# Kernel tuning notes

Hardware: AMD Instinct MI355X
Metric: run time of the kernel (lower is better)

The kernel has to match this reference:

```python
import jax, jax.numpy as jnp
import numpy as np

OUT = 7          # roi_align output_size
NUM_ANCHORS = 27 # 3 scales x 3 ratios x 3 angles
MAX_PROPOSALS = 100
RPN_STRIDE = 32


def conv2d(x, w, b, stride=1, pad=1):
    y = jax.lax.conv_general_dilated(
        x, w, (stride, stride), [(pad, pad), (pad, pad)],
        dimension_numbers=('NCHW', 'OIHW', 'NCHW'))
    return y + b[None, :, None, None]


def generate_anchors(H, W, stride):
    # matches CustomOrientedRPN.generate_anchors
    sx = np.arange(0, W * stride, stride, dtype=np.float32)
    sy = np.arange(0, H * stride, stride, dtype=np.float32)
    SY, SX = np.meshgrid(sy, sx, indexing='ij')
    shifts = np.stack([SX, SY], axis=-1).reshape(-1, 2)  # [HW,2]
    base = []
    for scale in (32.0, 64.0, 128.0):
        for ratio in (0.5, 1.0, 2.0):
            w = scale * ratio ** 0.5
            h = scale / ratio ** 0.5
            for angle in (0.0, 45.0, 90.0):
                base.append([w, h, angle])
    base = np.array(base, dtype=np.float32)  # [A,3]
    A = base.shape[0]
    anchors = np.concatenate(
        [np.repeat(shifts[:, None, :], A, axis=1),
         np.broadcast_to(base[None], (shifts.shape[0], A, 3))], axis=-1)
    return jnp.asarray(anchors.reshape(-1, 5))  # [HW*A, 5]


def rotated_roi_align(features, boxes, batch_idx):
    # Vectorized version of the per-box affine_grid + grid_sample loop
    # (align_corners=False semantics for both, zero padding for grid_sample).
    B, C, Hf, Wf = features.shape
    lin = (2.0 * jnp.arange(OUT, dtype=features.dtype) + 1.0) / OUT - 1.0
    ys, xs = jnp.meshgrid(lin, lin, indexing='ij')  # [7,7] base grid

    cx, cy, w, h, ang = (boxes[:, i] for i in range(5))
    ar = -ang * jnp.pi / 180.0
    c, s = jnp.cos(ar), jnp.sin(ar)
    t00 = w / Wf * c; t01 = -h / Hf * s; t02 = 2.0 * cx / Wf - 1.0
    t10 = w / Wf * s; t11 = h / Hf * c;  t12 = 2.0 * cy / Hf - 1.0
    gx = t00[:, None, None] * xs + t01[:, None, None] * ys + t02[:, None, None]  # [N,7,7]
    gy = t10[:, None, None] * xs + t11[:, None, None] * ys + t12[:, None, None]

    ix = ((gx + 1.0) * Wf - 1.0) / 2.0
    iy = ((gy + 1.0) * Hf - 1.0) / 2.0
    x0 = jnp.floor(ix); y0 = jnp.floor(iy)
    wx = ix - x0;       wy = iy - y0
    x0i = x0.astype(jnp.int32); y0i = y0.astype(jnp.int32)

    def gather(dx, dy, wgt):
        xi = x0i + dx; yi = y0i + dy
        valid = (xi >= 0) & (xi < Wf) & (yi >= 0) & (yi < Hf)
        xc = jnp.clip(xi, 0, Wf - 1)
        yc = jnp.clip(yi, 0, Hf - 1)
        def one(bi, yb, xb):
            return features[bi][:, yb, xb]  # [C,7,7]
        vals = jax.vmap(one)(batch_idx, yc, xc)  # [N,C,7,7]
        return vals * (wgt * valid)[:, None, :, :]

    return (gather(0, 0, (1 - wx) * (1 - wy)) + gather(1, 0, wx * (1 - wy)) +
            gather(0, 1, (1 - wx) * wy) + gather(1, 1, wx * wy))


def setup_inputs() -> dict:
    key = jax.random.key(0)
    ks = jax.random.split(key, 20)

    def w(k, shape):
        fan_in = int(np.prod(shape[1:]))
        return jax.random.normal(k, shape, jnp.float32) / np.sqrt(fan_in)

    C = 256; A = NUM_ANCHORS; NC = 5
    return {
        'images': jax.random.normal(ks[0], (8, 3, 1024, 1024), jnp.float32),
        'backbone_w': w(ks[1], (C, 3, 3, 3)),   'backbone_b': jnp.zeros((C,), jnp.float32),
        'rpn_conv_w': w(ks[2], (256, C, 3, 3)), 'rpn_conv_b': jnp.zeros((256,), jnp.float32),
        'obj_w': w(ks[3], (A, 256, 1, 1)),      'obj_b': jnp.zeros((A,), jnp.float32),
        'delta_w': w(ks[4], (A * 5, 256, 1, 1)) * 0.1, 'delta_b': jnp.zeros((A * 5,), jnp.float32),
        'fc1_w': w(ks[5], (1024, C * OUT * OUT)), 'fc1_b': jnp.zeros((1024,), jnp.float32),
        'fc2_w': w(ks[6], (1024, 1024)),          'fc2_b': jnp.zeros((1024,), jnp.float32),
        'cls_w': w(ks[7], (NC, 1024)),            'cls_b': jnp.zeros((NC,), jnp.float32),
        'bbox_w': w(ks[8], (5, 1024)),            'bbox_b': jnp.zeros((5,), jnp.float32),
    }


def reference(images, backbone_w, backbone_b, rpn_conv_w, rpn_conv_b,
              obj_w, obj_b, delta_w, delta_b,
              fc1_w, fc1_b, fc2_w, fc2_b, cls_w, cls_b, bbox_w, bbox_b):
    # backbone (stand-in: single stride-16 conv)
    f = conv2d(images, backbone_w, backbone_b, stride=16, pad=1)  # [B,256,64,64]
    B, C, H, W = f.shape
    # F.interpolate(scale_factor=0.5, bilinear, align_corners=False) == 2x2 mean
    f = f.reshape(B, C, H // 2, 2, W // 2, 2).mean(axis=(3, 5))   # [B,256,32,32]
    Hf, Wf = f.shape[2], f.shape[3]

    # RPN
    t = jax.nn.relu(conv2d(f, rpn_conv_w, rpn_conv_b, 1, 1))
    _logits = conv2d(t, obj_w, obj_b, 1, 0)  # computed as in original (unused downstream)
    deltas = conv2d(t, delta_w, delta_b, 1, 0)  # [B, A*5, Hf, Wf]
    A = NUM_ANCHORS
    deltas = deltas.reshape(B, A, 5, Hf, Wf).transpose(0, 3, 4, 1, 2).reshape(B, -1, 5)

    anchors = generate_anchors(Hf, Wf, RPN_STRIDE)  # [HW*A,5]
    acx, acy, aw, ah, aa = (anchors[:, i] for i in range(5))
    pcx = deltas[:, :, 0] * aw + acx
    pcy = deltas[:, :, 1] * ah + acy
    pw = jnp.exp(deltas[:, :, 2]) * aw
    ph = jnp.exp(deltas[:, :, 3]) * ah
    pa = aa + deltas[:, :, 4]
    proposals = jnp.stack([pcx, pcy, pw, ph, pa], axis=-1)  # [B, HW*A, 5]
    proposals = proposals[:, :MAX_PROPOSALS]                # p[:max_proposals]

    boxes = proposals.reshape(-1, 5)                        # [B*100, 5]
    batch_idx = jnp.repeat(jnp.arange(B), MAX_PROPOSALS)
    pooled = rotated_roi_align(f, boxes, batch_idx)         # [B*100, 256, 7, 7]

    x = pooled.reshape(pooled.shape[0], -1)
    x = jax.nn.relu(x @ fc1_w.T + fc1_b)
    x = jax.nn.relu(x @ fc2_w.T + fc2_b)
    class_logits = x @ cls_w.T + cls_b
    obb_preds = x @ bbox_w.T + bbox_b
    return class_logits, obb_preds
```

## Files before the change

### kernel.cpp

```cpp
#include <hip/hip_runtime.h>
#include <hip/hip_bf16.h>

using bf16 = __hip_bfloat16;

typedef __attribute__((ext_vector_type(8))) short bf16x8;
typedef __attribute__((ext_vector_type(4))) float f32x4;

__device__ __forceinline__ void async16(const void* g, void* l) {
  __builtin_amdgcn_global_load_lds(
      (const __attribute__((address_space(1))) unsigned int*)g,
      (__attribute__((address_space(3))) unsigned int*)l, 16, 0, 0);
}

__device__ __forceinline__ void store_o(float* C, size_t i, float v) { C[i] = v; }
__device__ __forceinline__ void store_o(bf16* C, size_t i, float v) {
  C[i] = __float2bfloat16(v);
}

__global__ __launch_bounds__(256) void k_backbone(const float* __restrict__ img,
    const float* __restrict__ w, const float* __restrict__ bias,
    float* __restrict__ f) {
  int blk = blockIdx.x;
  int x = blk & 31, y = (blk >> 5) & 31, b = blk >> 10;
  __shared__ float patch[4 * 27];
  int t = threadIdx.x;
  if (t < 108) {
    int kx = t % 3, ky = (t / 3) % 3, cin = (t / 9) % 3, sub = t / 27;
    int sy = sub >> 1, sx = sub & 1;
    int iy = (2 * y + sy) * 16 - 1 + ky;
    int ix = (2 * x + sx) * 16 - 1 + kx;
    float v = 0.f;
    if (iy >= 0 && ix >= 0)
      v = img[((size_t)(b * 3 + cin) * 1024 + iy) * 1024 + ix];
    patch[t] = v;
  }
  __syncthreads();
  int c = t;
  float wr[27];
#pragma unroll
  for (int k = 0; k < 27; ++k) wr[k] = w[c * 27 + k];
  float acc = 0.f;
#pragma unroll
  for (int sub = 0; sub < 4; ++sub)
#pragma unroll
    for (int k = 0; k < 27; ++k)
      acc += patch[sub * 27 + k] * wr[k];
  f[(size_t)blk * 256 + c] = acc * 0.25f + bias[c];
}

__global__ __launch_bounds__(256) void k_rpn(const float* __restrict__ f,
    const float* __restrict__ rpn_w, float* __restrict__ part) {
  int p = blockIdx.x;
  int kc = blockIdx.y;
  int x = p & 3, b = p >> 2;
  __shared__ float fpl[6][16];
  int tid = threadIdx.x;
  if (tid < 96) {
    int cin2 = tid & 15;
    int rc = tid >> 4;
    int row = rc / 3, col = rc % 3;
    int xc = x - 1 + col;
    float v = 0.f;
    if (xc >= 0)
      v = f[((size_t)(b * 32 + row) * 32 + xc) * 256 + kc * 16 + cin2];
    fpl[rc][cin2] = v;
  }
  __syncthreads();
  int c = tid;
  const float* wbase = rpn_w + (size_t)c * 2304 + kc * 144;
  float acc = 0.f;
#pragma unroll
  for (int cin2 = 0; cin2 < 16; ++cin2) {
    const float* wp = wbase + cin2 * 9;
    acc += fpl[0][cin2] * wp[3] + fpl[1][cin2] * wp[4]
         + fpl[2][cin2] * wp[5] + fpl[3][cin2] * wp[6]
         + fpl[4][cin2] * wp[7] + fpl[5][cin2] * wp[8];
  }
  part[((size_t)kc * 32 + p) * 256 + c] = acc;
}

__global__ __launch_bounds__(512) void k_delta(const float* __restrict__ part,
    const float* __restrict__ rpn_b,
    const float* __restrict__ dw, const float* __restrict__ db,
    float* __restrict__ boxes) {
  int p = blockIdx.x;
  int x = p & 3, b = p >> 2;
  __shared__ float tbuf[256];
  __shared__ float dvals[135];
  int tid = threadIdx.x;
  if (tid < 256) {
    float s = rpn_b[tid];
#pragma unroll
    for (int kc = 0; kc < 16; ++kc)
      s += part[((size_t)kc * 32 + p) * 256 + tid];
    tbuf[tid] = fmaxf(s, 0.f);
  }
  __syncthreads();
  if (tid < 270) {
    int o = tid >> 1, half = tid & 1;
    const float* wp = dw + (size_t)o * 256 + half * 128;
    const float* tp = tbuf + half * 128;
    float s = 0.f;
#pragma unroll 8
    for (int k = 0; k < 128; ++k) s += tp[k] * wp[k];
    s += __shfl_xor(s, 1, 64);
    if (half == 0) dvals[o] = s + db[o];
  }
  __syncthreads();
  if (tid < 27) {
    int i = x * 27 + tid;
    if (i < 100) {
      int a = tid;
      int si = a / 9, ri = (a / 3) % 3, ai = a % 3;
      float scale = 32.f * (float)(1 << si);
      float sr = (ri == 0) ? 0.70710678118654752f : (ri == 1 ? 1.0f : 1.41421356237309505f);
      float aw = scale * sr, ah = scale / sr;
      float aang = 45.f * (float)ai;
      float acx = 32.f * (float)x, acy = 0.f;
      float* bx = boxes + (size_t)(b * 100 + i) * 5;
      bx[0] = dvals[a * 5 + 0] * aw + acx;
      bx[1] = dvals[a * 5 + 1] * ah + acy;
      bx[2] = expf(dvals[a * 5 + 2]) * aw;
      bx[3] = expf(dvals[a * 5 + 3]) * ah;
      bx[4] = aang + dvals[a * 5 + 4];
    }
  }
}

__global__ __launch_bounds__(256) void k_roialign(const float* __restrict__ f,
    const float* __restrict__ boxes, bf16* __restrict__ pooled) {
  int n = blockIdx.x;
  int b = n / 100;
  __shared__ int six[49], siy[49];
  __shared__ float swx[49], swy[49];
  __shared__ float pool_s[12544];
  int tid = threadIdx.x;
  if (tid < 49) {
    float cx = boxes[n * 5 + 0], cy = boxes[n * 5 + 1];
    float w = boxes[n * 5 + 2], h = boxes[n * 5 + 3], ang = boxes[n * 5 + 4];
    float ar = -ang * 0.017453292519943295f;
    float cc = cosf(ar), ss = sinf(ar);
    float t00 = w * (1.f / 32.f) * cc, t01 = -h * (1.f / 32.f) * ss;
    float t02 = cx * (2.f / 32.f) - 1.f;
    float t10 = w * (1.f / 32.f) * ss, t11 = h * (1.f / 32.f) * cc;
    float t12 = cy * (2.f / 32.f) - 1.f;
    int py = tid / 7, px = tid - py * 7;
    float lx = (2.f * px + 1.f) * (1.f / 7.f) - 1.f;
    float ly = (2.f * py + 1.f) * (1.f / 7.f) - 1.f;
    float gx = t00 * lx + t01 * ly + t02;
    float gy = t10 * lx + t11 * ly + t12;
    float ix = ((gx + 1.f) * 32.f - 1.f) * 0.5f;
    float iy = ((gy + 1.f) * 32.f - 1.f) * 0.5f;
    float x0 = floorf(ix), y0 = floorf(iy);
    six[tid] = (int)x0; siy[tid] = (int)y0;
    swx[tid] = ix - x0; swy[tid] = iy - y0;
  }
  __syncthreads();
  const float* fb = f + (size_t)b * 262144;
  int c = tid;
  for (int bin = 0; bin < 49; ++bin) {
    int x0 = six[bin], y0 = siy[bin];
    float wx = swx[bin], wy = swy[bin];
    float acc = 0.f;
    if (x0 >= 0 && x0 < 32 && y0 >= 0 && y0 < 32)
      acc += fb[(y0 * 32 + x0) * 256 + c] * ((1.f - wx) * (1.f - wy));
    if (x0 + 1 >= 0 && x0 + 1 < 32 && y0 >= 0 && y0 < 32)
      acc += fb[(y0 * 32 + x0 + 1) * 256 + c] * (wx * (1.f - wy));
    if (x0 >= 0 && x0 < 32 && y0 + 1 >= 0 && y0 + 1 < 32)
      acc += fb[((y0 + 1) * 32 + x0) * 256 + c] * ((1.f - wx) * wy);
    if (x0 + 1 >= 0 && x0 + 1 < 32 && y0 + 1 >= 0 && y0 + 1 < 32)
      acc += fb[((y0 + 1) * 32 + x0 + 1) * 256 + c] * (wx * wy);
    pool_s[c * 49 + bin] = acc;
  }
  __syncthreads();
  bf16* po = pooled + (size_t)n * 12544;
  for (int k = tid; k < 12544; k += 256) po[k] = __float2bfloat16(pool_s[k]);
}

__device__ __forceinline__ unsigned int pk2(float a, float b) {
  unsigned int ua = __bfloat16_as_ushort(__float2bfloat16(a));
  unsigned int ub = __bfloat16_as_ushort(__float2bfloat16(b));
  return ua | (ub << 16);
}
__global__ __launch_bounds__(256) void k_cvt(const float* __restrict__ s,
    uint2* __restrict__ d, int n4) {
  int stride = gridDim.x * 256;
  for (int j = blockIdx.x * 256 + threadIdx.x; j < n4; j += stride) {
    float4 v = ((const float4*)s)[j];
    uint2 o;
    o.x = pk2(v.x, v.y);
    o.y = pk2(v.z, v.w);
    d[j] = o;
  }
}

__global__ __launch_bounds__(256) void k_gemm_bb(
    const unsigned short* __restrict__ A, const unsigned short* __restrict__ B,
    float* __restrict__ P, int M, int N, int K, int KC) {
  __shared__ unsigned short As[128 * 64];
  __shared__ unsigned short Bs[128 * 64];
  int t = threadIdx.x;
  int wv = t >> 6, ln = t & 63;
  int quad = ln >> 4, l15 = ln & 15;
  int wm = wv >> 1, wn = wv & 1;
  int n0 = blockIdx.x * 128, m0 = blockIdx.y * 128;
  int kbeg = blockIdx.z * KC;
  int kend = kbeg + KC; if (kend > K) kend = K;

  int srow = ln >> 3;
  int sg = (ln & 7) ^ srow;
  const unsigned short* Ap[4];
#pragma unroll
  for (int q = 0; q < 4; ++q) {
    int r = m0 + q * 32 + wv * 8 + srow;
    if (r > M - 1) r = M - 1;
    Ap[q] = A + (size_t)r * K + sg * 8;
  }
  const unsigned short* Bp[4];
#pragma unroll
  for (int c = 0; c < 4; ++c) {
    int r = n0 + wv * 32 + c * 8 + srow;
    Bp[c] = B + (size_t)r * K + sg * 8;
  }

  f32x4 acc[4][4];
#pragma unroll
  for (int mf = 0; mf < 4; ++mf)
#pragma unroll
    for (int nf = 0; nf < 4; ++nf) acc[mf][nf] = (f32x4){0.f, 0.f, 0.f, 0.f};

  for (int k0 = kbeg; k0 < kend; k0 += 64) {
    __syncthreads();
#pragma unroll
    for (int q = 0; q < 4; ++q)
      async16(Ap[q] + k0, &As[q * 2048 + wv * 512]);
#pragma unroll
    for (int c = 0; c < 4; ++c)
      async16(Bp[c] + k0, &Bs[wv * 2048 + c * 512]);
    __syncthreads();
#pragma unroll
    for (int ks = 0; ks < 2; ++ks) {
      bf16x8 a[4];
#pragma unroll
      for (int mf = 0; mf < 4; ++mf) {
        int row = wm * 64 + mf * 16 + l15;
        a[mf] = *(const bf16x8*)&As[row * 64 + (((ks * 4 + quad) ^ (l15 & 7)) * 8)];
      }
#pragma unroll
      for (int nf = 0; nf < 4; ++nf) {
        int brow = wn * 64 + nf * 16 + l15;
        bf16x8 b = *(const bf16x8*)&Bs[brow * 64 + (((ks * 4 + quad) ^ (l15 & 7)) * 8)];
#pragma unroll
        for (int mf = 0; mf < 4; ++mf)
          acc[mf][nf] = __builtin_amdgcn_mfma_f32_16x16x32_bf16(a[mf], b, acc[mf][nf], 0, 0, 0);
      }
    }
  }
#pragma unroll
  for (int nf = 0; nf < 4; ++nf) {
    int n = n0 + wn * 64 + nf * 16 + l15;
#pragma unroll
    for (int mf = 0; mf < 4; ++mf) {
#pragma unroll
      for (int r = 0; r < 4; ++r) {
        int m = m0 + wm * 64 + mf * 16 + quad * 4 + r;
        if (m < M) atomicAdd(&P[(size_t)m * N + n], acc[mf][nf][r]);
      }
    }
  }
}

template <typename OutT>
__global__ __launch_bounds__(256) void k_bias_relu(const float* __restrict__ P,
    const float* __restrict__ bias, OutT* __restrict__ C, int MN, int N) {
  int i = blockIdx.x * 256 + threadIdx.x;
  if (i * 4 >= MN) return;
  f32x4 s = *(const f32x4*)(P + (size_t)i * 4);
  int n = (i * 4) % N;
#pragma unroll
  for (int u = 0; u < 4; ++u)
    store_o(C, (size_t)i * 4 + u, fmaxf(s[u] + bias[n + u], 0.f));
}

__global__ __launch_bounds__(640) void k_heads(const float* __restrict__ x2,
    const float* __restrict__ cls_w, const float* __restrict__ cls_b,
    const float* __restrict__ bbox_w, const float* __restrict__ bbox_b,
    float* __restrict__ out) {
  int n = blockIdx.x;
  int wave = threadIdx.x >> 6;
  int lane = threadIdx.x & 63;
  const float* w = (wave < 5) ? (cls_w + (size_t)wave * 1024)
                              : (bbox_w + (size_t)(wave - 5) * 1024);
  const float* xr = x2 + (size_t)n * 1024;
  float s = 0.f;
  for (int k = lane; k < 1024; k += 64) s += xr[k] * w[k];
  for (int off = 32; off; off >>= 1) s += __shfl_down(s, off, 64);
  if (lane == 0) {
    int o = (wave < 5) ? wave : wave - 5;
    float bias = (wave < 5) ? cls_b[o] : bbox_b[o];
    int base = (wave < 5) ? 0 : 4000;
    out[base + n * 5 + o] = s + bias;
  }
}

extern "C" void kernel_launch(void* const* d_in, const int* in_sizes, int n_in,
                              void* d_out, int out_size, void* d_ws, size_t ws_size,
                              hipStream_t stream) {
  const float* images     = (const float*)d_in[0];
  const float* backbone_w = (const float*)d_in[1];
  const float* backbone_b = (const float*)d_in[2];
  const float* rpn_w      = (const float*)d_in[3];
  const float* rpn_b      = (const float*)d_in[4];
  const float* delta_w    = (const float*)d_in[7];
  const float* delta_b    = (const float*)d_in[8];
  const float* fc1_w      = (const float*)d_in[9];
  const float* fc1_b      = (const float*)d_in[10];
  const float* fc2_w      = (const float*)d_in[11];
  const float* fc2_b      = (const float*)d_in[12];
  const float* cls_w      = (const float*)d_in[13];
  const float* cls_b      = (const float*)d_in[14];
  const float* bbox_w     = (const float*)d_in[15];
  const float* bbox_b     = (const float*)d_in[16];

  char* ws = (char*)d_ws;
  bf16*  bw1    = (bf16*) ws;
  float* f      = (float*)ws;
  float* boxes  = (float*)(ws + 25690112);
  bf16*  pooled = (bf16*) (ws + 25706496);
  float* x2     = (float*)(ws + 25706496);
  bf16*  x1     = (bf16*) (ws + 45776896);
  float* P      = (float*)(ws + 47415296);
  bf16*  bw2    = (bf16*) (ws + 50692096);
  float* rpart  = P;

  k_backbone<<<8192, 256, 0, stream>>>(images, backbone_w, backbone_b, f);
  k_rpn<<<dim3(32, 16), 256, 0, stream>>>(f, rpn_w, rpart);
  k_delta<<<32, 512, 0, stream>>>(rpart, rpn_b, delta_w, delta_b, boxes);
  k_roialign<<<800, 256, 0, stream>>>(f, boxes, pooled);

  k_cvt<<<2048, 256, 0, stream>>>(fc1_w, (uint2*)bw1, 3211264);
  k_cvt<<<512, 256, 0, stream>>>(fc2_w, (uint2*)bw2, 262144);

  hipMemsetAsync(P, 0, 3276800, stream);
  k_gemm_bb<<<dim3(8, 7, 12), 256, 0, stream>>>(
      (const unsigned short*)pooled, (const unsigned short*)bw1, P,
      800, 1024, 12544, 1088);
  k_bias_relu<bf16><<<800, 256, 0, stream>>>(P, fc1_b, x1, 819200, 1024);

  hipMemsetAsync(P, 0, 3276800, stream);
  k_gemm_bb<<<dim3(8, 7, 8), 256, 0, stream>>>(
      (const unsigned short*)x1, (const unsigned short*)bw2, P,
      800, 1024, 1024, 128);
  k_bias_relu<float><<<800, 256, 0, stream>>>(P, fc2_b, x2, 819200, 1024);

  k_heads<<<800, 640, 0, stream>>>(x2, cls_w, cls_b, bbox_w, bbox_b, (float*)d_out);
}
```

Before: 374.0 us.

## Double-buffer GEMM LDS loads, fuse weight conversion with zeroing, drop memsets

The bf16 GEMM now double-buffers its LDS tiles. The next K-slice's async global-to-LDS loads are issued before computing on the current slice, with explicit vmcnt waits and barriers. The two weight-conversion kernels and the first memset are merged into one kernel, and the second memset is folded into the first bias-relu kernel, which zeroes the accumulator after reading it. The split-K count for fc1 goes from 12 to 14 chunks of 896. The changes remove launch overhead and hide load latency, at the cost of double the LDS use and more atomics.

```diff
diff --git a/kernel.cpp b/kernel.cpp
--- a/kernel.cpp
+++ b/kernel.cpp
@@ -182,23 +182,34 @@
   unsigned int ub = __bfloat16_as_ushort(__float2bfloat16(b));
   return ua | (ub << 16);
 }
-__global__ __launch_bounds__(256) void k_cvt(const float* __restrict__ s,
-    uint2* __restrict__ d, int n4) {
+__global__ __launch_bounds__(256) void k_cvtz(const float* __restrict__ s1,
+    const float* __restrict__ s2, uint2* __restrict__ d1,
+    uint2* __restrict__ d2, f32x4* __restrict__ Pz) {
+  const int N1 = 3211264;
+  const int N2 = 262144;
+  const int NZ = 204800;
   int stride = gridDim.x * 256;
-  for (int j = blockIdx.x * 256 + threadIdx.x; j < n4; j += stride) {
-    float4 v = ((const float4*)s)[j];
-    uint2 o;
-    o.x = pk2(v.x, v.y);
-    o.y = pk2(v.z, v.w);
-    d[j] = o;
+  for (int j = blockIdx.x * 256 + threadIdx.x; j < N1 + N2 + NZ; j += stride) {
+    if (j < N1) {
+      float4 v = ((const float4*)s1)[j];
+      uint2 o; o.x = pk2(v.x, v.y); o.y = pk2(v.z, v.w);
+      d1[j] = o;
+    } else if (j < N1 + N2) {
+      int i = j - N1;
+      float4 v = ((const float4*)s2)[i];
+      uint2 o; o.x = pk2(v.x, v.y); o.y = pk2(v.z, v.w);
+      d2[i] = o;
+    } else {
+      Pz[j - N1 - N2] = (f32x4){0.f, 0.f, 0.f, 0.f};
+    }
   }
 }
 
 __global__ __launch_bounds__(256) void k_gemm_bb(
     const unsigned short* __restrict__ A, const unsigned short* __restrict__ B,
     float* __restrict__ P, int M, int N, int K, int KC) {
-  __shared__ unsigned short As[128 * 64];
-  __shared__ unsigned short Bs[128 * 64];
+  __shared__ unsigned short As[2][128 * 64];
+  __shared__ unsigned short Bs[2][128 * 64];
   int t = threadIdx.x;
   int wv = t >> 6, ln = t & 63;
   int quad = ln >> 4, l15 = ln & 15;
@@ -229,32 +240,50 @@
 #pragma unroll
     for (int nf = 0; nf < 4; ++nf) acc[mf][nf] = (f32x4){0.f, 0.f, 0.f, 0.f};
 
+#pragma unroll
+  for (int q = 0; q < 4; ++q)
+    async16(Ap[q] + kbeg, &As[0][q * 2048 + wv * 512]);
+#pragma unroll
+  for (int c = 0; c < 4; ++c)
+    async16(Bp[c] + kbeg, &Bs[0][wv * 2048 + c * 512]);
+
+  int cur = 0;
   for (int k0 = kbeg; k0 < kend; k0 += 64) {
-    __syncthreads();
-#pragma unroll
-    for (int q = 0; q < 4; ++q)
-      async16(Ap[q] + k0, &As[q * 2048 + wv * 512]);
-#pragma unroll
-    for (int c = 0; c < 4; ++c)
-      async16(Bp[c] + k0, &Bs[wv * 2048 + c * 512]);
-    __syncthreads();
+    int k1 = k0 + 64;
+    if (k1 < kend) {
+#pragma unroll
+      for (int q = 0; q < 4; ++q)
+        async16(Ap[q] + k1, &As[cur ^ 1][q * 2048 + wv * 512]);
+#pragma unroll
+      for (int c = 0; c < 4; ++c)
+        async16(Bp[c] + k1, &Bs[cur ^ 1][wv * 2048 + c * 512]);
+      asm volatile("s_waitcnt vmcnt(8)" ::: "memory");
+    } else {
+      asm volatile("s_waitcnt vmcnt(0)" ::: "memory");
+    }
+    __builtin_amdgcn_s_barrier();
+    __builtin_amdgcn_sched_barrier(0);
 #pragma unroll
     for (int ks = 0; ks < 2; ++ks) {
       bf16x8 a[4];
 #pragma unroll
       for (int mf = 0; mf < 4; ++mf) {
         int row = wm * 64 + mf * 16 + l15;
-        a[mf] = *(const bf16x8*)&As[row * 64 + (((ks * 4 + quad) ^ (l15 & 7)) * 8)];
+        a[mf] = *(const bf16x8*)&As[cur][row * 64 + (((ks * 4 + quad) ^ (l15 & 7)) * 8)];
       }
 #pragma unroll
       for (int nf = 0; nf < 4; ++nf) {
         int brow = wn * 64 + nf * 16 + l15;
-        bf16x8 b = *(const bf16x8*)&Bs[brow * 64 + (((ks * 4 + quad) ^ (l15 & 7)) * 8)];
+        bf16x8 b = *(const bf16x8*)&Bs[cur][brow * 64 + (((ks * 4 + quad) ^ (l15 & 7)) * 8)];
 #pragma unroll
         for (int mf = 0; mf < 4; ++mf)
           acc[mf][nf] = __builtin_amdgcn_mfma_f32_16x16x32_bf16(a[mf], b, acc[mf][nf], 0, 0, 0);
       }
     }
+    __builtin_amdgcn_sched_barrier(0);
+    asm volatile("" ::: "memory");
+    __builtin_amdgcn_s_barrier();
+    cur ^= 1;
   }
 #pragma unroll
   for (int nf = 0; nf < 4; ++nf) {
@@ -270,8 +299,8 @@
   }
 }
 
-template <typename OutT>
-__global__ __launch_bounds__(256) void k_bias_relu(const float* __restrict__ P,
+template <typename OutT, bool RZ>
+__global__ __launch_bounds__(256) void k_bias_relu(float* __restrict__ P,
     const float* __restrict__ bias, OutT* __restrict__ C, int MN, int N) {
   int i = blockIdx.x * 256 + threadIdx.x;
   if (i * 4 >= MN) return;
@@ -280,6 +309,7 @@
 #pragma unroll
   for (int u = 0; u < 4; ++u)
     store_o(C, (size_t)i * 4 + u, fmaxf(s[u] + bias[n + u], 0.f));
+  if (RZ) *(f32x4*)(P + (size_t)i * 4) = (f32x4){0.f, 0.f, 0.f, 0.f};
 }
 
 __global__ __launch_bounds__(640) void k_heads(const float* __restrict__ x2,
@@ -338,20 +368,18 @@
   k_delta<<<32, 512, 0, stream>>>(rpart, rpn_b, delta_w, delta_b, boxes);
   k_roialign<<<800, 256, 0, stream>>>(f, boxes, pooled);
 
-  k_cvt<<<2048, 256, 0, stream>>>(fc1_w, (uint2*)bw1, 3211264);
-  k_cvt<<<512, 256, 0, stream>>>(fc2_w, (uint2*)bw2, 262144);
-
-  hipMemsetAsync(P, 0, 3276800, stream);
-  k_gemm_bb<<<dim3(8, 7, 12), 256, 0, stream>>>(
+  k_cvtz<<<2048, 256, 0, stream>>>(fc1_w, fc2_w, (uint2*)bw1, (uint2*)bw2,
+                                   (f32x4*)P);
+
+  k_gemm_bb<<<dim3(8, 7, 14), 256, 0, stream>>>(
       (const unsigned short*)pooled, (const unsigned short*)bw1, P,
-      800, 1024, 12544, 1088);
-  k_bias_relu<bf16><<<800, 256, 0, stream>>>(P, fc1_b, x1, 819200, 1024);
-
-  hipMemsetAsync(P, 0, 3276800, stream);
+      800, 1024, 12544, 896);
+  k_bias_relu<bf16, true><<<800, 256, 0, stream>>>(P, fc1_b, x1, 819200, 1024);
+
   k_gemm_bb<<<dim3(8, 7, 8), 256, 0, stream>>>(
       (const unsigned short*)x1, (const unsigned short*)bw2, P,
       800, 1024, 1024, 128);
-  k_bias_relu<float><<<800, 256, 0, stream>>>(P, fc2_b, x2, 819200, 1024);
+  k_bias_relu<float, false><<<800, 256, 0, stream>>>(P, fc2_b, x2, 819200, 1024);
 
   k_heads<<<800, 640, 0, stream>>>(x2, cls_w, cls_b, bbox_w, bbox_b, (float*)d_out);
 }
```

After: 364.6 us. 1.03x faster.
